# Kernel tuning notes

Measured on AMD Instinct MI355X. Metric: run time of the kernel, lower is better.

Reference implementation:

```python
import jax, jax.numpy as jnp
import numpy as np

B, N, E, H = 4, 8192, 256, 8
EXP = 4  # params['num_layers'] -> MLP expansion
HID = EXP * E
EPS = 1e-5


def _layernorm(x, w, b):
    mu = jnp.mean(x, axis=-1, keepdims=True)
    var = jnp.mean(jnp.square(x - mu), axis=-1, keepdims=True)
    return (x - mu) * jax.lax.rsqrt(var + EPS) * w + b


def _mish(x):
    return x * jnp.tanh(jax.nn.softplus(x))


def setup_inputs() -> dict:
    key = jax.random.key(0)
    ks = jax.random.split(key, 12)
    s = 0.02
    return {
        "x": jax.random.normal(ks[0], (B, N, E), dtype=jnp.float32),
        "ln1_w": jnp.ones((E,), jnp.float32),
        "ln1_b": jnp.zeros((E,), jnp.float32),
        "Wq": jax.random.normal(ks[1], (E, E), jnp.float32) * s,
        "bq": jnp.zeros((E,), jnp.float32),
        "Wk": jax.random.normal(ks[2], (E, E), jnp.float32) * s,
        "bk": jnp.zeros((E,), jnp.float32),
        "Wv": jax.random.normal(ks[3], (E, E), jnp.float32) * s,
        "bv": jnp.zeros((E,), jnp.float32),
        "Wp": jax.random.normal(ks[4], (E, E), jnp.float32) * s,
        "bp": jnp.zeros((E,), jnp.float32),
        "ln2_w": jnp.ones((E,), jnp.float32),
        "ln2_b": jnp.zeros((E,), jnp.float32),
        "W1": jax.random.normal(ks[5], (HID, E), jnp.float32) * s,
        "b1": jnp.zeros((HID,), jnp.float32),
        "W2": jax.random.normal(ks[6], (E, HID), jnp.float32) * s,
        "b2": jnp.zeros((E,), jnp.float32),
    }


def _msa(x, Wq, bq, Wk, bk, Wv, bv, Wp, bp):
    b, n, e = x.shape
    d = n // H  # sequence-chunk per head (faithful to source rearrange)
    q = (x @ Wq.T + bq).reshape(b, H, d, e)
    k = (x @ Wk.T + bk).reshape(b, H, d, e)
    v = (x @ Wv.T + bv).reshape(b, H, d, e)
    scale = jnp.sqrt(jnp.float32(E))
    energy = jnp.einsum('bhie,bhke->bhik', q, k)  # (b,H,d,d)
    att = jax.nn.softmax(energy, axis=3) / scale
    o = jnp.einsum('bhik,bhke->bhie', att, v).reshape(b, n, e)
    return o @ Wp.T + bp


def reference(x, ln1_w, ln1_b, Wq, bq, Wk, bk, Wv, bv, Wp, bp,
              ln2_w, ln2_b, W1, b1, W2, b2):
    # pre-LN attention block + residual
    x1 = _msa(_layernorm(x, ln1_w, ln1_b), Wq, bq, Wk, bk, Wv, bv, Wp, bp) + x
    # pre-LN MLP (Mish after both linears, per source) + residual
    h = _layernorm(x1, ln2_w, ln2_b)
    h = _mish(h @ W1.T + b1)
    h = _mish(h @ W2.T + b2)
    return h + x1
```

## Files before the change

kernel.cpp:

```cpp
#include <hip/hip_runtime.h>

typedef float  f32x4  __attribute__((ext_vector_type(4)));
typedef float  f4v    __attribute__((ext_vector_type(4)));
typedef __bf16 bf16x8 __attribute__((ext_vector_type(8)));
typedef __bf16 bf16x4 __attribute__((ext_vector_type(4)));
typedef unsigned short ushort_t;

#define AS1 __attribute__((address_space(1)))
#define AS3 __attribute__((address_space(3)))

static __device__ __forceinline__ void gload_lds16(const void* g, void* l) {
  __builtin_amdgcn_global_load_lds((const AS1 void*)g, (AS3 void*)l, 16, 0, 0);
}

static __device__ __forceinline__ float mishf(float x) {
  float t = __expf(x);
  float u = t * (t + 2.f);
  float y = x * __fdividef(u, u + 2.f);
  return (x > 15.f) ? x : y;
}

__global__ __launch_bounds__(256) void packw(
    const float* __restrict__ Wq, const float* __restrict__ Wk,
    const float* __restrict__ Wv, const float* __restrict__ Wp,
    const float* __restrict__ W1, const float* __restrict__ W2,
    __bf16* __restrict__ out)
{
  const int t = blockIdx.x * 256 + threadIdx.x;
  const int e0 = t * 8;
  int rel, K; const float* src;
  if      (e0 < 196608) { rel = e0;          K = 256;  src = nullptr; }
  else if (e0 < 262144) { rel = e0 - 196608; K = 256;  src = Wp; }
  else if (e0 < 524288) { rel = e0 - 262144; K = 256;  src = W1; }
  else                  { rel = e0 - 524288; K = 1024; src = W2; }
  const int percb = (K >> 8) * 8192;
  const int cb = rel / percb;  const int r1 = rel % percb;
  const int c  = r1 / 8192;    const int r2 = r1 % 8192;
  const int u  = r2 / 1024;    const int r3 = r2 % 1024;
  const int n  = r3 / 512;     const int l  = (r3 % 512) >> 3;
  const int col = cb * 32 + n * 16 + (l & 15);
  const int k   = c * 256 + u * 32 + ((l >> 4) << 3);
  const float* sp;
  if (e0 < 196608) {
    const float* qkvsrc = (col < 256) ? Wq : (col < 512 ? Wk : Wv);
    sp = qkvsrc + (size_t)(col & 255) * 256 + k;
  } else {
    sp = src + (size_t)col * K + k;
  }
  const f4v a = *(const f4v*)(sp);
  const f4v b = *(const f4v*)(sp + 4);
  bf16x8 o;
  #pragma unroll
  for (int j = 0; j < 4; ++j) { o[j] = (__bf16)a[j]; o[4 + j] = (__bf16)b[j]; }
  *(bf16x8*)(out + e0) = o;
}

__global__ void packb(const float* __restrict__ a, const float* __restrict__ b,
                      const float* __restrict__ c, float* __restrict__ o) {
  int i = threadIdx.x;
  o[i] = (i < 256) ? a[i] : (i < 512 ? b[i - 256] : c[i - 512]);
}

template<int BM, int NT, int KC, int ACT, int RES, int OUTBF,
         int LNSTAGE, int LNFUSE, int RESBF>
__global__ __launch_bounds__(512, 2) void bgemm(
    const __bf16* __restrict__ A, const float* __restrict__ Xf,
    const __bf16* __restrict__ Wg, const float* __restrict__ bias,
    const void* __restrict__ res, const float* __restrict__ lnw,
    const float* __restrict__ lnb, void* __restrict__ out,
    void* __restrict__ out2, int ldo)
{
  constexpr int K  = KC * 256;
  constexpr int MR = BM / 32;
  __shared__ __bf16 Ab[BM * 256];
  __shared__ float redS[64][4];
  __shared__ float redQ[64][4];
  const int tid = threadIdx.x, l = tid & 63, w = tid >> 6;
  const int wr = w >> 2, wc = w & 3;
  constexpr int nwg = (32768 / BM) * NT;
  const int wg = (blockIdx.x & 7) * (nwg / 8) + (blockIdx.x >> 3);
  const int mt = wg / NT, nt = wg % NT;
  const int row0 = mt * BM;
  const int col0 = nt * 256 + wc * 64;
  const int cb0 = nt * 8 + wc * 2;

  auto stageA = [&](int c) {
    #pragma unroll
    for (int j = 0; j < BM / 16; ++j) {
      const int s = j * 512 + tid;
      const int r = s >> 5, q = s & 31;
      gload_lds16(A + (size_t)(row0 + r) * K + c * 256 + ((q ^ (r & 7)) << 3),
                  &Ab[s << 3]);
    }
  };

  auto ldBu = [&](bf16x8* d, int c, int u) {
    const __bf16* wp0 = Wg + ((size_t)cb0 * KC + c) * 8192 + (((u << 1) * 64 + l) << 3);
    const __bf16* wp1 = wp0 + (size_t)KC * 8192;
    d[0] = *(const bf16x8*)(wp0);
    d[1] = *(const bf16x8*)(wp0 + 512);
    d[2] = *(const bf16x8*)(wp1);
    d[3] = *(const bf16x8*)(wp1 + 512);
  };

  f32x4 acc[MR][4] = {};

  if constexpr (LNSTAGE) {
    const int q = tid & 31;
    const f4v ga0 = *(const f4v*)(lnw + q * 8);
    const f4v ga1 = *(const f4v*)(lnw + q * 8 + 4);
    const f4v bb0 = *(const f4v*)(lnb + q * 8);
    const f4v bb1 = *(const f4v*)(lnb + q * 8 + 4);
    #pragma unroll
    for (int j = 0; j < BM / 16; ++j) {
      const int s = j * 512 + tid, r = s >> 5;
      const float* xp = Xf + (size_t)(row0 + r) * 256 + q * 8;
      const f4v xa = *(const f4v*)xp;
      const f4v xb = *(const f4v*)(xp + 4);
      float s1 = xa[0] + xa[1] + xa[2] + xa[3] + xb[0] + xb[1] + xb[2] + xb[3];
      float s2 = xa[0]*xa[0] + xa[1]*xa[1] + xa[2]*xa[2] + xa[3]*xa[3]
               + xb[0]*xb[0] + xb[1]*xb[1] + xb[2]*xb[2] + xb[3]*xb[3];
      #pragma unroll
      for (int mk = 1; mk < 32; mk <<= 1) {
        s1 += __shfl_xor(s1, mk); s2 += __shfl_xor(s2, mk);
      }
      const float mu = s1 * (1.f / 256.f);
      const float rs = rsqrtf(s2 * (1.f / 256.f) - mu * mu + 1e-5f);
      bf16x8 o;
      #pragma unroll
      for (int i = 0; i < 4; ++i) {
        o[i]     = (__bf16)((xa[i] - mu) * rs * ga0[i] + bb0[i]);
        o[4 + i] = (__bf16)((xb[i] - mu) * rs * ga1[i] + bb1[i]);
      }
      *(bf16x8*)&Ab[((r << 5) | (q ^ (r & 7))) << 3] = o;
    }
    __syncthreads();
  } else {
    stageA(0);
    asm volatile("s_waitcnt vmcnt(0)" ::: "memory");
    __builtin_amdgcn_s_barrier();
  }

  for (int c = 0;;) {
    bf16x8 b0[4], b1[4];
    ldBu(b0, c, 0);
    #pragma unroll
    for (int u = 0; u < 8; ++u) {
      if (u + 1 < 8) ldBu((u & 1) ? b0 : b1, c, u + 1);
      const bf16x8* bu = (u & 1) ? b1 : b0;
      bf16x8 af[MR];
      #pragma unroll
      for (int m = 0; m < MR; ++m) {
        const int r = wr * (BM / 2) + m * 16 + (l & 15);
        const int q = ((u << 2) | (l >> 4)) ^ (r & 7);
        af[m] = *(const bf16x8*)&Ab[((r << 5) | q) << 3];
      }
      #pragma unroll
      for (int m = 0; m < MR; ++m)
        #pragma unroll
        for (int n = 0; n < 4; ++n)
          acc[m][n] = __builtin_amdgcn_mfma_f32_16x16x32_bf16(af[m], bu[n], acc[m][n], 0, 0, 0);
    }
    if (++c == KC) break;
    __syncthreads();
    stageA(c);
    asm volatile("s_waitcnt vmcnt(0)" ::: "memory");
    __builtin_amdgcn_s_barrier();
  }

  float bs[4];
  #pragma unroll
  for (int n = 0; n < 4; ++n) bs[n] = bias[col0 + n * 16 + (l & 15)];

  if constexpr (LNFUSE) {
    #pragma unroll
    for (int m = 0; m < MR; ++m) {
      #pragma unroll
      for (int r = 0; r < 4; ++r) {
        const int row = row0 + wr * (BM / 2) + m * 16 + ((l >> 4) << 2) + r;
        const float* rp = (const float*)res + (size_t)row * ldo + col0;
        float s1v = 0.f, s2v = 0.f;
        #pragma unroll
        for (int n = 0; n < 4; ++n) {
          float v = acc[m][n][r] + bs[n] + rp[n * 16 + (l & 15)];
          acc[m][n][r] = v;
          s1v += v; s2v += v * v;
        }
        #pragma unroll
        for (int mk = 1; mk < 16; mk <<= 1) {
          s1v += __shfl_xor(s1v, mk); s2v += __shfl_xor(s2v, mk);
        }
        if ((l & 15) == 0) { redS[row - row0][wc] = s1v; redQ[row - row0][wc] = s2v; }
      }
    }
    __syncthreads();
    float wlv[4], blv[4];
    #pragma unroll
    for (int n = 0; n < 4; ++n) {
      wlv[n] = lnw[col0 + n * 16 + (l & 15)];
      blv[n] = lnb[col0 + n * 16 + (l & 15)];
    }
    #pragma unroll
    for (int m = 0; m < MR; ++m) {
      #pragma unroll
      for (int r = 0; r < 4; ++r) {
        const int row = row0 + wr * (BM / 2) + m * 16 + ((l >> 4) << 2) + r;
        const int lrow = row - row0;
        const f4v ss = *(const f4v*)redS[lrow];
        const f4v qq = *(const f4v*)redQ[lrow];
        const float mu = (ss[0] + ss[1] + ss[2] + ss[3]) * (1.f / 256.f);
        const float var = (qq[0] + qq[1] + qq[2] + qq[3]) * (1.f / 256.f) - mu * mu;
        const float rsv = rsqrtf(var + 1e-5f);
        __bf16* o1 = (__bf16*)out  + (size_t)row * ldo + col0;
        __bf16* o2 = (__bf16*)out2 + (size_t)row * ldo + col0;
        #pragma unroll
        for (int n = 0; n < 4; ++n) {
          const float v = acc[m][n][r];
          o1[n * 16 + (l & 15)] = (__bf16)v;
          o2[n * 16 + (l & 15)] = (__bf16)((v - mu) * rsv * wlv[n] + blv[n]);
        }
      }
    }
  } else {
    #pragma unroll
    for (int m = 0; m < MR; ++m) {
      #pragma unroll
      for (int r = 0; r < 4; ++r) {
        const int row = row0 + wr * (BM / 2) + m * 16 + ((l >> 4) << 2) + r;
        float v[4];
        #pragma unroll
        for (int n = 0; n < 4; ++n) {
          v[n] = acc[m][n][r] + bs[n];
          if (ACT) v[n] = mishf(v[n]);
        }
        if (RES) {
          if constexpr (RESBF) {
            const __bf16* rp = (const __bf16*)res + (size_t)row * ldo + col0;
            #pragma unroll
            for (int n = 0; n < 4; ++n) v[n] += (float)rp[n * 16 + (l & 15)];
          } else {
            const float* rp = (const float*)res + (size_t)row * ldo + col0;
            #pragma unroll
            for (int n = 0; n < 4; ++n) v[n] += rp[n * 16 + (l & 15)];
          }
        }
        if (OUTBF) {
          __bf16* op = (__bf16*)out + (size_t)row * ldo + col0;
          #pragma unroll
          for (int n = 0; n < 4; ++n) op[n * 16 + (l & 15)] = (__bf16)v[n];
        } else {
          float* op = (float*)out + (size_t)row * ldo + col0;
          #pragma unroll
          for (int n = 0; n < 4; ++n) op[n * 16 + (l & 15)] = v[n];
        }
      }
    }
  }
}

__global__ __launch_bounds__(512) void attn_fwd(
    const __bf16* __restrict__ QKV, __bf16* __restrict__ Om)
{
  __shared__ __bf16 Ks[2][32][256];
  __shared__ __bf16 Vs[2][256][32];
  __shared__ __bf16 Ps[8][16][32];
  const int tid = threadIdx.x, l = tid & 63, w = tid >> 6;
  const int wgs = (blockIdx.x & 7) * 32 + (blockIdx.x >> 3);
  const int bh = wgs >> 3, qt = wgs & 7;
  const size_t rbase = (size_t)bh * 1024 * 768;
  const int qr0 = qt * 128 + w * 16;

  bf16x8 qf[8];
  {
    const __bf16* qp = QKV + rbase + (size_t)(qr0 + (l & 15)) * 768 + ((l >> 4) << 3);
    #pragma unroll
    for (int s = 0; s < 8; ++s) qf[s] = *(const bf16x8*)(qp + s * 32);
  }
  f32x4 acc[16] = {};
  float lacc[4] = {0.f, 0.f, 0.f, 0.f};

  const int kec = tid & 31, kr_ = tid >> 5;
  const int vp = tid & 15, vc = tid >> 4;
  const __bf16* gK = QKV + 256 + rbase + kec * 8;
  const __bf16* gV = QKV + 512 + rbase + vc * 8;

  uint4 rk0, rk1, rv0, rv1;
  auto ldKV = [&](int kt) {
    const __bf16* k0 = gK + (size_t)(kt * 32 + kr_) * 768;
    rk0 = *(const uint4*)k0;
    rk1 = *(const uint4*)(k0 + 16 * 768);
    const __bf16* v0 = gV + (size_t)(kt * 32 + vp * 2) * 768;
    rv0 = *(const uint4*)v0;
    rv1 = *(const uint4*)(v0 + 768);
  };
  auto wrKV = [&](int buf) {
    char* kb = (char*)&Ks[buf][0][0];
    const int a0 = (kr_ * 512 + kec * 16) ^ ((kr_ & 15) << 4);
    const int a1 = ((kr_ + 16) * 512 + kec * 16) ^ (((kr_ + 16) & 15) << 4);
    *(uint4*)(kb + a0) = rk0;
    *(uint4*)(kb + a1) = rk1;
    const ushort_t* s0 = (const ushort_t*)&rv0;
    const ushort_t* s1 = (const ushort_t*)&rv1;
    #pragma unroll
    for (int i = 0; i < 8; ++i) {
      unsigned pk = (unsigned)s0[i] | ((unsigned)s1[i] << 16);
      *(unsigned*)&Vs[buf][vc * 8 + i][vp * 2] = pk;
    }
  };

  ldKV(0); wrKV(0);
  __syncthreads();
  int cur = 0;
  for (int kt = 0;;) {
    if (kt + 1 < 32) ldKV(kt + 1);
    f32x4 S[2] = {};
    const char* kbase = (const char*)&Ks[cur][0][0];
    #pragma unroll
    for (int t = 0; t < 2; ++t) {
      const int kcol = t * 16 + (l & 15);
      const int swz = (kcol & 15) << 4;
      #pragma unroll
      for (int s = 0; s < 8; ++s) {
        uint4 kf = *(const uint4*)(kbase + ((kcol * 512 + s * 64 + ((l >> 4) << 4)) ^ swz));
        S[t] = __builtin_amdgcn_mfma_f32_16x16x32_bf16(qf[s], __builtin_bit_cast(bf16x8, kf), S[t], 0, 0, 0);
      }
    }
    #pragma unroll
    for (int t = 0; t < 2; ++t)
      #pragma unroll
      for (int r = 0; r < 4; ++r) {
        float p = __expf(S[t][r]);
        lacc[r] += p;
        Ps[w][((l >> 4) << 2) + r][t * 16 + (l & 15)] = (__bf16)p;
      }
    bf16x8 pf = *(const bf16x8*)&Ps[w][l & 15][(l >> 4) << 3];
    #pragma unroll
    for (int n = 0; n < 16; ++n) {
      uint4 vf = *(const uint4*)&Vs[cur][n * 16 + (l & 15)][(l >> 4) << 3];
      acc[n] = __builtin_amdgcn_mfma_f32_16x16x32_bf16(pf, __builtin_bit_cast(bf16x8, vf), acc[n], 0, 0, 0);
    }
    if (++kt == 32) break;
    wrKV(cur ^ 1);
    __syncthreads();
    cur ^= 1;
  }
  f32x4 inv;
  #pragma unroll
  for (int r = 0; r < 4; ++r) {
    float s = lacc[r];
    s += __shfl_xor(s, 1); s += __shfl_xor(s, 2);
    s += __shfl_xor(s, 4); s += __shfl_xor(s, 8);
    inv[r] = 1.f / (16.f * s);
  }
  __bf16* op = Om + (size_t)(bh * 1024 + qr0 + ((l >> 4) << 2)) * 256 + (l & 15);
  #pragma unroll
  for (int n = 0; n < 16; ++n)
    #pragma unroll
    for (int r = 0; r < 4; ++r)
      op[(size_t)r * 256 + n * 16] = (__bf16)(acc[n][r] * inv[r]);
}

extern "C" void kernel_launch(void* const* d_in, const int* in_sizes, int n_in,
                              void* d_out, int out_size, void* d_ws, size_t ws_size,
                              hipStream_t stream)
{
  const float* x    = (const float*)d_in[0];
  const float* ln1w = (const float*)d_in[1];
  const float* ln1b = (const float*)d_in[2];
  const float* Wq   = (const float*)d_in[3];
  const float* bq   = (const float*)d_in[4];
  const float* Wk   = (const float*)d_in[5];
  const float* bk   = (const float*)d_in[6];
  const float* Wv   = (const float*)d_in[7];
  const float* bv   = (const float*)d_in[8];
  const float* Wp   = (const float*)d_in[9];
  const float* bp   = (const float*)d_in[10];
  const float* ln2w = (const float*)d_in[11];
  const float* ln2b = (const float*)d_in[12];
  const float* W1   = (const float*)d_in[13];
  const float* b1   = (const float*)d_in[14];
  const float* W2   = (const float*)d_in[15];
  const float* b2   = (const float*)d_in[16];

  char* ws = (char*)d_ws;
  __bf16* wb   = (__bf16*)(ws);
  float*  bqkv = (float*)(ws + 1572864);
  __bf16* y    = (__bf16*)(ws + 2097152);
  __bf16* qkv  = (__bf16*)(ws + 18874368);
  __bf16* x1b  = (__bf16*)(ws + 18874368);
  __bf16* hb   = (__bf16*)(ws + 52428800);
  __bf16* h1   = (__bf16*)(ws + 69206016);
  __bf16* ao   = y;
  float*  outp = (float*)d_out;

  packw<<<384, 256, 0, stream>>>(Wq, Wk, Wv, Wp, W1, W2, wb);
  packb<<<1, 768, 0, stream>>>(bq, bk, bv, bqkv);
  bgemm<128, 3, 1, 0, 0, 1, 1, 0, 0><<<768, 512, 0, stream>>>(
      nullptr, x, wb, bqkv, nullptr, ln1w, ln1b, qkv, nullptr, 768);
  attn_fwd<<<256, 512, 0, stream>>>(qkv, ao);
  bgemm<64, 1, 1, 0, 1, 0, 0, 1, 0><<<512, 512, 0, stream>>>(
      ao, nullptr, wb + 196608, bp, x, ln2w, ln2b, x1b, hb, 256);
  bgemm<128, 4, 1, 1, 0, 1, 0, 0, 0><<<1024, 512, 0, stream>>>(
      hb, nullptr, wb + 262144, b1, nullptr, nullptr, nullptr, h1, nullptr, 1024);
  bgemm<64, 1, 4, 1, 1, 0, 0, 0, 1><<<512, 512, 0, stream>>>(
      h1, nullptr, wb + 524288, b2, x1b, nullptr, nullptr, outp, nullptr, 256);
}
```

Baseline: 196.0 us.

## Fuse MLP up- and down-projection into one kernel keeping hidden chunk in LDS

Replaces the two MLP GEMM launches with a single kernel. Each workgroup loads a 64-row tile of the normalized activations once, computes the 1024-wide hidden layer in four 256-column chunks with Mish applied, stores each chunk to LDS and immediately accumulates it into the second projection. The bias, Mish and residual epilogue are applied at the end. This removes the 64MB bf16 hidden-activation round trip through global memory and one launch, in exchange for smaller row tiles (64 rows), weights reread per workgroup, and extra barriers between chunks.

```diff
diff --git a/kernel.cpp b/kernel.cpp
--- a/kernel.cpp
+++ b/kernel.cpp
@@ -258,6 +258,121 @@
   }
 }
 
+__global__ __launch_bounds__(512, 2) void mlpf(
+    const __bf16* __restrict__ Hb, const __bf16* __restrict__ W1p,
+    const __bf16* __restrict__ W2p, const float* __restrict__ b1,
+    const float* __restrict__ b2, const __bf16* __restrict__ x1b,
+    float* __restrict__ out)
+{
+  __shared__ __bf16 Ab[64 * 256];
+  __shared__ __bf16 Hc[64 * 256];
+  const int tid = threadIdx.x, l = tid & 63, w = tid >> 6;
+  const int wr = w >> 2, wc = w & 3;
+  const int wg = (blockIdx.x & 7) * 64 + (blockIdx.x >> 3);
+  const int row0 = wg * 64;
+
+  #pragma unroll
+  for (int j = 0; j < 4; ++j) {
+    const int s = j * 512 + tid, r = s >> 5, q = s & 31;
+    gload_lds16(Hb + (size_t)(row0 + r) * 256 + ((q ^ (r & 7)) << 3),
+                &Ab[s << 3]);
+  }
+
+  auto ldB = [&](bf16x8* d, const __bf16* base, int cb0, int KC, int kc, int u) {
+    const __bf16* wp0 = base + ((size_t)cb0 * KC + kc) * 8192 + (((u << 1) * 64 + l) << 3);
+    const __bf16* wp1 = wp0 + (size_t)KC * 8192;
+    d[0] = *(const bf16x8*)(wp0);
+    d[1] = *(const bf16x8*)(wp0 + 512);
+    d[2] = *(const bf16x8*)(wp1);
+    d[3] = *(const bf16x8*)(wp1 + 512);
+  };
+
+  f32x4 acc2[2][4] = {};
+
+  asm volatile("s_waitcnt vmcnt(0)" ::: "memory");
+  __builtin_amdgcn_s_barrier();
+
+  for (int c = 0; c < 4; ++c) {
+    if (c) __syncthreads();
+    f32x4 acc1[2][4] = {};
+    {
+      bf16x8 b0[4], b1v[4];
+      ldB(b0, W1p, c * 8 + wc * 2, 1, 0, 0);
+      #pragma unroll
+      for (int u = 0; u < 8; ++u) {
+        if (u + 1 < 8) ldB((u & 1) ? b0 : b1v, W1p, c * 8 + wc * 2, 1, 0, u + 1);
+        const bf16x8* bu = (u & 1) ? b1v : b0;
+        bf16x8 af[2];
+        #pragma unroll
+        for (int m = 0; m < 2; ++m) {
+          const int r = wr * 32 + m * 16 + (l & 15);
+          const int q = ((u << 2) | (l >> 4)) ^ (r & 7);
+          af[m] = *(const bf16x8*)&Ab[((r << 5) | q) << 3];
+        }
+        #pragma unroll
+        for (int m = 0; m < 2; ++m)
+          #pragma unroll
+          for (int n = 0; n < 4; ++n)
+            acc1[m][n] = __builtin_amdgcn_mfma_f32_16x16x32_bf16(af[m], bu[n], acc1[m][n], 0, 0, 0);
+      }
+    }
+    #pragma unroll
+    for (int n = 0; n < 4; ++n) {
+      const int col = wc * 64 + n * 16 + (l & 15);
+      const float bb = b1[c * 256 + col];
+      #pragma unroll
+      for (int m = 0; m < 2; ++m)
+        #pragma unroll
+        for (int r = 0; r < 4; ++r) {
+          const int row = wr * 32 + m * 16 + ((l >> 4) << 2) + r;
+          const int q = (col >> 3) ^ (row & 7);
+          Hc[(((row << 5) | q) << 3) + (col & 7)] = (__bf16)mishf(acc1[m][n][r] + bb);
+        }
+    }
+    __syncthreads();
+    {
+      bf16x8 b0[4], b1v[4];
+      ldB(b0, W2p, wc * 2, 4, c, 0);
+      #pragma unroll
+      for (int u = 0; u < 8; ++u) {
+        if (u + 1 < 8) ldB((u & 1) ? b0 : b1v, W2p, wc * 2, 4, c, u + 1);
+        const bf16x8* bu = (u & 1) ? b1v : b0;
+        bf16x8 af[2];
+        #pragma unroll
+        for (int m = 0; m < 2; ++m) {
+          const int r = wr * 32 + m * 16 + (l & 15);
+          const int q = ((u << 2) | (l >> 4)) ^ (r & 7);
+          af[m] = *(const bf16x8*)&Hc[((r << 5) | q) << 3];
+        }
+        #pragma unroll
+        for (int m = 0; m < 2; ++m)
+          #pragma unroll
+          for (int n = 0; n < 4; ++n)
+            acc2[m][n] = __builtin_amdgcn_mfma_f32_16x16x32_bf16(af[m], bu[n], acc2[m][n], 0, 0, 0);
+      }
+    }
+  }
+
+  const int col0 = wc * 64;
+  float bs[4];
+  #pragma unroll
+  for (int n = 0; n < 4; ++n) bs[n] = b2[col0 + n * 16 + (l & 15)];
+  #pragma unroll
+  for (int m = 0; m < 2; ++m) {
+    #pragma unroll
+    for (int r = 0; r < 4; ++r) {
+      const int row = row0 + wr * 32 + m * 16 + ((l >> 4) << 2) + r;
+      const __bf16* rp = x1b + (size_t)row * 256 + col0;
+      float* op = out + (size_t)row * 256 + col0;
+      #pragma unroll
+      for (int n = 0; n < 4; ++n) {
+        float v = mishf(acc2[m][n][r] + bs[n]) + (float)rp[n * 16 + (l & 15)];
+        op[n * 16 + (l & 15)] = v;
+      }
+    }
+  }
+}
+
 __global__ __launch_bounds__(512) void attn_fwd(
     const __bf16* __restrict__ QKV, __bf16* __restrict__ Om)
 {
@@ -389,7 +504,6 @@
   __bf16* qkv  = (__bf16*)(ws + 18874368);
   __bf16* x1b  = (__bf16*)(ws + 18874368);
   __bf16* hb   = (__bf16*)(ws + 52428800);
-  __bf16* h1   = (__bf16*)(ws + 69206016);
   __bf16* ao   = y;
   float*  outp = (float*)d_out;
 
@@ -400,8 +514,5 @@
   attn_fwd<<<256, 512, 0, stream>>>(qkv, ao);
   bgemm<64, 1, 1, 0, 1, 0, 0, 1, 0><<<512, 512, 0, stream>>>(
       ao, nullptr, wb + 196608, bp, x, ln2w, ln2b, x1b, hb, 256);
-  bgemm<128, 4, 1, 1, 0, 1, 0, 0, 0><<<1024, 512, 0, stream>>>(
-      hb, nullptr, wb + 262144, b1, nullptr, nullptr, nullptr, h1, nullptr, 1024);
-  bgemm<64, 1, 4, 1, 1, 0, 0, 0, 1><<<512, 512, 0, stream>>>(
-      h1, nullptr, wb + 524288, b2, x1b, nullptr, nullptr, outp, nullptr, 256);
-}
+  mlpf<<<512, 512, 0, stream>>>(hb, wb + 262144, wb + 524288, b1, b2, x1b, outp);
+}
```

Result: slower. 209.3 us (+6.7%).
